# Kernel optimization log

Measured on AMD Instinct MI355X. Metric: run time of the kernel, lower is better.

## Reference

```python
import jax, jax.numpy as jnp
import numpy as np

B, T, D_MEM, D_Q, D_ATT, C_LOC, K = 64, 2000, 512, 1024, 128, 32, 31


def setup_inputs() -> dict:
    key = jax.random.key(0)
    ks = jax.random.split(key, 9)
    return {
        "attention_hidden_state": jax.random.normal(ks[0], (B, 1, D_Q), jnp.float32),
        "memory": jax.random.normal(ks[1], (B, T, D_MEM), jnp.float32),
        "processed_memory": jax.random.normal(ks[2], (B, T, D_ATT), jnp.float32),
        "attention_weights": jax.random.uniform(ks[3], (B, 2, T), jnp.float32),
        "Wq": jax.random.normal(ks[4], (D_Q, D_ATT), jnp.float32) * 0.02,
        "Wconv": jax.random.normal(ks[5], (C_LOC, 2, K), jnp.float32) * 0.1,
        "bconv": jax.random.normal(ks[6], (C_LOC,), jnp.float32) * 0.01,
        "Wloc": jax.random.normal(ks[7], (C_LOC, D_ATT), jnp.float32) * 0.1,
        "v": jax.random.normal(ks[8], (D_ATT,), jnp.float32) * 0.1,
    }


def reference(attention_hidden_state, memory, processed_memory, attention_weights,
              Wq, Wconv, bconv, Wloc, v):
    # query projection: [B,1,1024] @ [1024,128] -> [B,1,128]
    processed_query = jnp.einsum("bqi,io->bqo", attention_hidden_state, Wq)
    # location conv: [B,2,T] -> [B,32,T], 'same' padding (k=31, pad=15)
    loc = jax.lax.conv_general_dilated(
        attention_weights, Wconv, window_strides=(1,), padding=[(15, 15)],
        dimension_numbers=("NCH", "OIH", "NCH"))
    loc = loc + bconv[None, :, None]
    # transpose to [B,T,32] then project to [B,T,128]
    processed_loc = jnp.einsum("bct,co->bto", loc, Wloc)
    # energies: v . tanh(q + loc + mem) -> [B,T]
    energies = jnp.einsum("btd,d->bt", jnp.tanh(processed_query + processed_loc + processed_memory), v)
    new_weights = jax.nn.softmax(energies, axis=1)
    # context: [B,T] x [B,T,D] -> [B,D]
    attention_context = jnp.einsum("bt,btd->bd", new_weights, memory)
    return attention_context, new_weights
```

## Files before the change

kernel.cpp:

```cpp
#include <hip/hip_runtime.h>
#include <hip/hip_bf16.h>

#define B 64
#define T 2000
#define D_MEM 512
#define D_Q 1024
#define D_ATT 128
#define C_LOC 32
#define K 31

#define WS_PQ       0
#define WS_ENERGY   (WS_PQ + B*D_ATT)
#define NCHUNK      20
#define TCHUNK      (T / NCHUNK)
#define WS_PARTIAL  (WS_ENERGY + B*T)

__device__ __forceinline__ float tanh_fast(float x) {
    float e = __expf(2.f * x);
    return 1.f - 2.f / (e + 1.f);
}

__global__ __launch_bounds__(512) void pq_kernel(const float* __restrict__ h,
                                                 const float* __restrict__ Wq,
                                                 float* __restrict__ pq) {
    int b = blockIdx.x;
    int tid = threadIdx.x;
    int ty = tid >> 7;
    int d  = tid & 127;
    __shared__ float sh[D_Q];
    __shared__ float red[4][D_ATT];
    const float* hb = h + (size_t)b * D_Q;
    if (tid < D_Q / 4) ((float4*)sh)[tid] = ((const float4*)hb)[tid];
    __syncthreads();
    float acc = 0.f;
    int ibeg = ty * 256;
#pragma unroll 8
    for (int i2 = 0; i2 < 256; ++i2) {
        int i = ibeg + i2;
        acc = fmaf(sh[i], Wq[(size_t)i * D_ATT + d], acc);
    }
    red[ty][d] = acc;
    __syncthreads();
    if (ty == 0)
        pq[b * D_ATT + d] = red[0][d] + red[1][d] + red[2][d] + red[3][d];
}

#define CH 40
#define TPT 5
__global__ __launch_bounds__(256) void energy_kernel(const float* __restrict__ aw,
                              const float* __restrict__ pmem,
                              const float* __restrict__ pq,
                              const float* __restrict__ Wconv,
                              const float* __restrict__ bconv,
                              const float* __restrict__ Wloc,
                              const float* __restrict__ v,
                              float* __restrict__ energies) {
    const int b  = blockIdx.y;
    const int t0 = blockIdx.x * CH;
    const int tid = threadIdx.x;

    __shared__ float s_aw[2][CH + K - 1];
    __shared__ float s_wc[2 * K * C_LOC];
    __shared__ float s_loc[CH][C_LOC];
    __shared__ float s_pq[D_ATT];

    for (int j = tid; j < 2 * (CH + K - 1); j += 256) {
        int i = j / (CH + K - 1), o = j % (CH + K - 1);
        int t = t0 - (K / 2) + o;
        s_aw[i][o] = (t >= 0 && t < T) ? aw[((size_t)b * 2 + i) * T + t] : 0.f;
    }
    for (int j = tid; j < C_LOC * 2 * K; j += 256) {
        int c = j / (2 * K), r = j % (2 * K);
        int i = r / K, k = r % K;
        s_wc[(i * K + k) * C_LOC + c] = Wconv[j];
    }
    if (tid < D_ATT) s_pq[tid] = pq[b * D_ATT + tid];
    __syncthreads();

    {
        int g = tid >> 5, c = tid & 31;
        float bc = bconv[c];
        float acc[TPT];
#pragma unroll
        for (int j = 0; j < TPT; ++j) acc[j] = bc;
#pragma unroll
        for (int i = 0; i < 2; ++i) {
#pragma unroll
            for (int k = 0; k < K; ++k) {
                float wv = s_wc[(i * K + k) * C_LOC + c];
#pragma unroll
                for (int j = 0; j < TPT; ++j)
                    acc[j] = fmaf(s_aw[i][g + 8 * j + k], wv, acc[j]);
            }
        }
#pragma unroll
        for (int j = 0; j < TPT; ++j) s_loc[g + 8 * j][c] = acc[j];
    }
    __syncthreads();

    int g = tid >> 5, dd = tid & 31;
    float4 pqv = ((const float4*)s_pq)[dd];
    float4 vv  = ((const float4*)v)[dd];
    float4 pl[TPT];
#pragma unroll
    for (int j = 0; j < TPT; ++j) pl[j] = make_float4(0.f, 0.f, 0.f, 0.f);
#pragma unroll
    for (int c = 0; c < C_LOC; ++c) {
        float4 w = ((const float4*)(Wloc + c * D_ATT))[dd];
#pragma unroll
        for (int j = 0; j < TPT; ++j) {
            float l = s_loc[g + 8 * j][c];
            pl[j].x = fmaf(l, w.x, pl[j].x);
            pl[j].y = fmaf(l, w.y, pl[j].y);
            pl[j].z = fmaf(l, w.z, pl[j].z);
            pl[j].w = fmaf(l, w.w, pl[j].w);
        }
    }
#pragma unroll
    for (int j = 0; j < TPT; ++j) {
        int t = t0 + g + 8 * j;
        float4 pm = ((const float4*)(pmem + ((size_t)b * T + t) * D_ATT))[dd];
        float e = vv.x * tanh_fast(pqv.x + pl[j].x + pm.x)
                + vv.y * tanh_fast(pqv.y + pl[j].y + pm.y)
                + vv.z * tanh_fast(pqv.z + pl[j].z + pm.z)
                + vv.w * tanh_fast(pqv.w + pl[j].w + pm.w);
#pragma unroll
        for (int off = 16; off >= 1; off >>= 1)
            e += __shfl_xor(e, off);
        if (dd == 0) energies[(size_t)b * T + t] = e;
    }
}

__global__ __launch_bounds__(256) void softmax_kernel(const float* __restrict__ energies,
                               float* __restrict__ weights) {
    int b = blockIdx.x, tid = threadIdx.x;
    const float* e = energies + (size_t)b * T;
    float vals[8];
    float m = -1e30f;
#pragma unroll
    for (int j = 0; j < 8; ++j) {
        int t = j * 256 + tid;
        vals[j] = (t < T) ? e[t] : -1e30f;
        m = fmaxf(m, vals[j]);
    }
    __shared__ float smax[4], ssum[4];
    int wid = tid >> 6, lane = tid & 63;
#pragma unroll
    for (int off = 32; off >= 1; off >>= 1) m = fmaxf(m, __shfl_xor(m, off));
    if (lane == 0) smax[wid] = m;
    __syncthreads();
    m = fmaxf(fmaxf(smax[0], smax[1]), fmaxf(smax[2], smax[3]));

    float s = 0.f;
#pragma unroll
    for (int j = 0; j < 8; ++j) {
        int t = j * 256 + tid;
        vals[j] = (t < T) ? __expf(vals[j] - m) : 0.f;
        s += vals[j];
    }
#pragma unroll
    for (int off = 32; off >= 1; off >>= 1) s += __shfl_xor(s, off);
    if (lane == 0) ssum[wid] = s;
    __syncthreads();
    s = ssum[0] + ssum[1] + ssum[2] + ssum[3];
    float inv = 1.f / s;
#pragma unroll
    for (int j = 0; j < 8; ++j) {
        int t = j * 256 + tid;
        if (t < T) weights[(size_t)b * T + t] = vals[j] * inv;
    }
}

__global__ __launch_bounds__(128) void ctx_partial_kernel(const float* __restrict__ memory,
                                   const float* __restrict__ weights,
                                   float* __restrict__ partial) {
    int b = blockIdx.y, s = blockIdx.x;
    int dq = threadIdx.x;
    int tbeg = s * TCHUNK;
    __shared__ float sw[TCHUNK];
    const float* w = weights + (size_t)b * T;
    for (int j = threadIdx.x; j < TCHUNK; j += 128) sw[j] = w[tbeg + j];
    __syncthreads();
    const float4* mem4 = (const float4*)(memory + (size_t)b * T * D_MEM);
    float4 acc = {0.f, 0.f, 0.f, 0.f};
#pragma unroll 10
    for (int j = 0; j < TCHUNK; ++j) {
        float wt = sw[j];
        float4 mv = mem4[(size_t)(tbeg + j) * (D_MEM / 4) + dq];
        acc.x = fmaf(wt, mv.x, acc.x);
        acc.y = fmaf(wt, mv.y, acc.y);
        acc.z = fmaf(wt, mv.z, acc.z);
        acc.w = fmaf(wt, mv.w, acc.w);
    }
    ((float4*)(partial + ((size_t)s * B + b) * D_MEM))[dq] = acc;
}

__global__ __launch_bounds__(256) void ctx_reduce_kernel(const float* __restrict__ partial,
                                  float* __restrict__ ctx) {
    int idx = blockIdx.x * 256 + threadIdx.x;
    float acc = 0.f;
#pragma unroll
    for (int s = 0; s < NCHUNK; ++s)
        acc += partial[(size_t)s * B * D_MEM + idx];
    ctx[idx] = acc;
}

extern "C" void kernel_launch(void* const* d_in, const int* in_sizes, int n_in,
                              void* d_out, int out_size, void* d_ws, size_t ws_size,
                              hipStream_t stream) {
    const float* hidden = (const float*)d_in[0];
    const float* memory = (const float*)d_in[1];
    const float* pmem   = (const float*)d_in[2];
    const float* aw     = (const float*)d_in[3];
    const float* Wq     = (const float*)d_in[4];
    const float* Wconv  = (const float*)d_in[5];
    const float* bconv  = (const float*)d_in[6];
    const float* Wloc   = (const float*)d_in[7];
    const float* v      = (const float*)d_in[8];

    float* out_ctx = (float*)d_out;
    float* out_w   = (float*)d_out + B * D_MEM;

    float* ws       = (float*)d_ws;
    float* pq       = ws + WS_PQ;
    float* energies = ws + WS_ENERGY;
    float* partial  = ws + WS_PARTIAL;

    pq_kernel<<<B, 512, 0, stream>>>(hidden, Wq, pq);
    energy_kernel<<<dim3(T / CH, B), 256, 0, stream>>>(aw, pmem, pq, Wconv, bconv,
                                                       Wloc, v, energies);
    softmax_kernel<<<B, 256, 0, stream>>>(energies, out_w);
    ctx_partial_kernel<<<dim3(NCHUNK, B), 128, 0, stream>>>(memory, out_w, partial);
    ctx_reduce_kernel<<<(B * D_MEM) / 256, 256, 0, stream>>>(partial, out_ctx);
}
```

Before: 523.0 us.

## Fuse energy, softmax numerator and context accumulation into one kernel

Merges the energy, softmax and context-partial kernels into one kernel per (batch, 100-step chunk). It computes exp(energy) without subtracting the max, accumulates per-chunk sums and unnormalized context partials, and then normalizes both outputs in a small finalize kernel. This removes the round trips through global memory for energies and weights and cuts the launch count from five to three. In exchange it drops max-subtraction, which risks overflow if energies are large. Larger chunks also mean fewer blocks and heavier per-thread register use.

After: 508.2 us. 2.8% less time.

```diff
diff --git a/kernel.cpp b/kernel.cpp
--- a/kernel.cpp
+++ b/kernel.cpp
@@ -9,11 +9,15 @@
 #define C_LOC 32
 #define K 31
 
-#define WS_PQ       0
-#define WS_ENERGY   (WS_PQ + B*D_ATT)
-#define NCHUNK      20
-#define TCHUNK      (T / NCHUNK)
-#define WS_PARTIAL  (WS_ENERGY + B*T)
+#define CH2 100
+#define NCH2 (T / CH2)
+#define TPG 13
+#define NPART (NCH2 * 2)
+
+#define WS_PQ    0
+#define WS_EXPW  (WS_PQ + B * D_ATT)
+#define WS_SUMS  (WS_EXPW + B * T)
+#define WS_PART  (WS_SUMS + B * NCH2)
 
 __device__ __forceinline__ float tanh_fast(float x) {
     float e = __expf(2.f * x);
@@ -45,33 +49,33 @@
         pq[b * D_ATT + d] = red[0][d] + red[1][d] + red[2][d] + red[3][d];
 }
 
-#define CH 40
-#define TPT 5
-__global__ __launch_bounds__(256) void energy_kernel(const float* __restrict__ aw,
-                              const float* __restrict__ pmem,
-                              const float* __restrict__ pq,
-                              const float* __restrict__ Wconv,
-                              const float* __restrict__ bconv,
-                              const float* __restrict__ Wloc,
-                              const float* __restrict__ v,
-                              float* __restrict__ energies) {
-    const int b  = blockIdx.y;
-    const int t0 = blockIdx.x * CH;
+__global__ __launch_bounds__(256) void mega_kernel(
+    const float* __restrict__ aw, const float* __restrict__ pmem,
+    const float* __restrict__ pq, const float* __restrict__ Wconv,
+    const float* __restrict__ bconv, const float* __restrict__ Wloc,
+    const float* __restrict__ v, const float* __restrict__ memory,
+    float* __restrict__ expw, float* __restrict__ sums,
+    float* __restrict__ partial) {
+    const int s = blockIdx.x, b = blockIdx.y;
+    const int t0 = s * CH2;
     const int tid = threadIdx.x;
 
-    __shared__ float s_aw[2][CH + K - 1];
+    __shared__ float s_aw[2][CH2 + K - 1];
     __shared__ float s_wc[2 * K * C_LOC];
-    __shared__ float s_loc[CH][C_LOC];
+    __shared__ float s_loc[CH2 + 4][C_LOC];
     __shared__ float s_pq[D_ATT];
-
-    for (int j = tid; j < 2 * (CH + K - 1); j += 256) {
-        int i = j / (CH + K - 1), o = j % (CH + K - 1);
+    __shared__ float s_e[CH2];
+    __shared__ float s_red[2];
+
+    const int AWW = CH2 + K - 1;
+    for (int j = tid; j < 2 * AWW; j += 256) {
+        int i = j / AWW, o = j - i * AWW;
         int t = t0 - (K / 2) + o;
         s_aw[i][o] = (t >= 0 && t < T) ? aw[((size_t)b * 2 + i) * T + t] : 0.f;
     }
     for (int j = tid; j < C_LOC * 2 * K; j += 256) {
-        int c = j / (2 * K), r = j % (2 * K);
-        int i = r / K, k = r % K;
+        int c = j / (2 * K), r = j - c * 2 * K;
+        int i = r / K, k = r - i * K;
         s_wc[(i * K + k) * C_LOC + c] = Wconv[j];
     }
     if (tid < D_ATT) s_pq[tid] = pq[b * D_ATT + tid];
@@ -80,129 +84,118 @@
     {
         int g = tid >> 5, c = tid & 31;
         float bc = bconv[c];
-        float acc[TPT];
-#pragma unroll
-        for (int j = 0; j < TPT; ++j) acc[j] = bc;
+        float acc[TPG];
+#pragma unroll
+        for (int j = 0; j < TPG; ++j) acc[j] = bc;
 #pragma unroll
         for (int i = 0; i < 2; ++i) {
 #pragma unroll
             for (int k = 0; k < K; ++k) {
                 float wv = s_wc[(i * K + k) * C_LOC + c];
 #pragma unroll
-                for (int j = 0; j < TPT; ++j)
+                for (int j = 0; j < TPG; ++j)
                     acc[j] = fmaf(s_aw[i][g + 8 * j + k], wv, acc[j]);
             }
         }
 #pragma unroll
-        for (int j = 0; j < TPT; ++j) s_loc[g + 8 * j][c] = acc[j];
-    }
-    __syncthreads();
-
-    int g = tid >> 5, dd = tid & 31;
-    float4 pqv = ((const float4*)s_pq)[dd];
-    float4 vv  = ((const float4*)v)[dd];
-    float4 pl[TPT];
-#pragma unroll
-    for (int j = 0; j < TPT; ++j) pl[j] = make_float4(0.f, 0.f, 0.f, 0.f);
-#pragma unroll
-    for (int c = 0; c < C_LOC; ++c) {
-        float4 w = ((const float4*)(Wloc + c * D_ATT))[dd];
-#pragma unroll
-        for (int j = 0; j < TPT; ++j) {
-            float l = s_loc[g + 8 * j][c];
-            pl[j].x = fmaf(l, w.x, pl[j].x);
-            pl[j].y = fmaf(l, w.y, pl[j].y);
-            pl[j].z = fmaf(l, w.z, pl[j].z);
-            pl[j].w = fmaf(l, w.w, pl[j].w);
-        }
-    }
-#pragma unroll
-    for (int j = 0; j < TPT; ++j) {
-        int t = t0 + g + 8 * j;
-        float4 pm = ((const float4*)(pmem + ((size_t)b * T + t) * D_ATT))[dd];
-        float e = vv.x * tanh_fast(pqv.x + pl[j].x + pm.x)
-                + vv.y * tanh_fast(pqv.y + pl[j].y + pm.y)
-                + vv.z * tanh_fast(pqv.z + pl[j].z + pm.z)
-                + vv.w * tanh_fast(pqv.w + pl[j].w + pm.w);
-#pragma unroll
-        for (int off = 16; off >= 1; off >>= 1)
-            e += __shfl_xor(e, off);
-        if (dd == 0) energies[(size_t)b * T + t] = e;
-    }
-}
-
-__global__ __launch_bounds__(256) void softmax_kernel(const float* __restrict__ energies,
-                               float* __restrict__ weights) {
+        for (int j = 0; j < TPG; ++j) s_loc[g + 8 * j][c] = acc[j];
+    }
+    __syncthreads();
+
+    {
+        int g = tid >> 5, dd = tid & 31;
+        float4 pqv = ((const float4*)s_pq)[dd];
+        float4 vv  = ((const float4*)v)[dd];
+        float4 pl[TPG];
+#pragma unroll
+        for (int j = 0; j < TPG; ++j) pl[j] = make_float4(0.f, 0.f, 0.f, 0.f);
+#pragma unroll
+        for (int c = 0; c < C_LOC; ++c) {
+            float4 w = ((const float4*)(Wloc + c * D_ATT))[dd];
+#pragma unroll
+            for (int j = 0; j < TPG; ++j) {
+                float l = s_loc[g + 8 * j][c];
+                pl[j].x = fmaf(l, w.x, pl[j].x);
+                pl[j].y = fmaf(l, w.y, pl[j].y);
+                pl[j].z = fmaf(l, w.z, pl[j].z);
+                pl[j].w = fmaf(l, w.w, pl[j].w);
+            }
+        }
+#pragma unroll
+        for (int j = 0; j < TPG; ++j) {
+            int tl = g + 8 * j;
+            if (tl < CH2) {
+                int t = t0 + tl;
+                float4 pm = ((const float4*)(pmem + ((size_t)b * T + t) * D_ATT))[dd];
+                float e = vv.x * tanh_fast(pqv.x + pl[j].x + pm.x)
+                        + vv.y * tanh_fast(pqv.y + pl[j].y + pm.y)
+                        + vv.z * tanh_fast(pqv.z + pl[j].z + pm.z)
+                        + vv.w * tanh_fast(pqv.w + pl[j].w + pm.w);
+#pragma unroll
+                for (int off = 16; off >= 1; off >>= 1)
+                    e += __shfl_xor(e, off);
+                if (dd == 0) s_e[tl] = __expf(e);
+            }
+        }
+    }
+    __syncthreads();
+
+    if (tid < 128) {
+        float vsum = (tid < CH2) ? s_e[tid] : 0.f;
+        if (tid < CH2) expw[(size_t)b * T + t0 + tid] = vsum;
+        float r = vsum;
+#pragma unroll
+        for (int off = 32; off >= 1; off >>= 1) r += __shfl_xor(r, off);
+        if ((tid & 63) == 0) s_red[tid >> 6] = r;
+    }
+    __syncthreads();
+    if (tid == 0) sums[b * NCH2 + s] = s_red[0] + s_red[1];
+
+    {
+        int dq = tid & 127, h = tid >> 7;
+        const float4* mem4 =
+            (const float4*)(memory + ((size_t)b * T + t0 + h * 50) * D_MEM);
+        float4 acc = {0.f, 0.f, 0.f, 0.f};
+#pragma unroll 10
+        for (int j = 0; j < 50; ++j) {
+            float wt = s_e[h * 50 + j];
+            float4 mv = mem4[(size_t)j * (D_MEM / 4) + dq];
+            acc.x = fmaf(wt, mv.x, acc.x);
+            acc.y = fmaf(wt, mv.y, acc.y);
+            acc.z = fmaf(wt, mv.z, acc.z);
+            acc.w = fmaf(wt, mv.w, acc.w);
+        }
+        ((float4*)(partial + ((size_t)(s * 2 + h) * B + b) * D_MEM))[dq] = acc;
+    }
+}
+
+__global__ __launch_bounds__(256) void finalize_kernel(
+    const float* __restrict__ expw, const float* __restrict__ sums,
+    const float* __restrict__ partial, float* __restrict__ out_w,
+    float* __restrict__ out_ctx) {
     int b = blockIdx.x, tid = threadIdx.x;
-    const float* e = energies + (size_t)b * T;
-    float vals[8];
-    float m = -1e30f;
-#pragma unroll
-    for (int j = 0; j < 8; ++j) {
-        int t = j * 256 + tid;
-        vals[j] = (t < T) ? e[t] : -1e30f;
-        m = fmaxf(m, vals[j]);
-    }
-    __shared__ float smax[4], ssum[4];
-    int wid = tid >> 6, lane = tid & 63;
-#pragma unroll
-    for (int off = 32; off >= 1; off >>= 1) m = fmaxf(m, __shfl_xor(m, off));
-    if (lane == 0) smax[wid] = m;
-    __syncthreads();
-    m = fmaxf(fmaxf(smax[0], smax[1]), fmaxf(smax[2], smax[3]));
-
-    float s = 0.f;
-#pragma unroll
-    for (int j = 0; j < 8; ++j) {
-        int t = j * 256 + tid;
-        vals[j] = (t < T) ? __expf(vals[j] - m) : 0.f;
-        s += vals[j];
-    }
-#pragma unroll
-    for (int off = 32; off >= 1; off >>= 1) s += __shfl_xor(s, off);
-    if (lane == 0) ssum[wid] = s;
-    __syncthreads();
-    s = ssum[0] + ssum[1] + ssum[2] + ssum[3];
-    float inv = 1.f / s;
-#pragma unroll
-    for (int j = 0; j < 8; ++j) {
-        int t = j * 256 + tid;
-        if (t < T) weights[(size_t)b * T + t] = vals[j] * inv;
-    }
-}
-
-__global__ __launch_bounds__(128) void ctx_partial_kernel(const float* __restrict__ memory,
-                                   const float* __restrict__ weights,
-                                   float* __restrict__ partial) {
-    int b = blockIdx.y, s = blockIdx.x;
-    int dq = threadIdx.x;
-    int tbeg = s * TCHUNK;
-    __shared__ float sw[TCHUNK];
-    const float* w = weights + (size_t)b * T;
-    for (int j = threadIdx.x; j < TCHUNK; j += 128) sw[j] = w[tbeg + j];
-    __syncthreads();
-    const float4* mem4 = (const float4*)(memory + (size_t)b * T * D_MEM);
-    float4 acc = {0.f, 0.f, 0.f, 0.f};
-#pragma unroll 10
-    for (int j = 0; j < TCHUNK; ++j) {
-        float wt = sw[j];
-        float4 mv = mem4[(size_t)(tbeg + j) * (D_MEM / 4) + dq];
-        acc.x = fmaf(wt, mv.x, acc.x);
-        acc.y = fmaf(wt, mv.y, acc.y);
-        acc.z = fmaf(wt, mv.z, acc.z);
-        acc.w = fmaf(wt, mv.w, acc.w);
-    }
-    ((float4*)(partial + ((size_t)s * B + b) * D_MEM))[dq] = acc;
-}
-
-__global__ __launch_bounds__(256) void ctx_reduce_kernel(const float* __restrict__ partial,
-                                  float* __restrict__ ctx) {
-    int idx = blockIdx.x * 256 + threadIdx.x;
-    float acc = 0.f;
-#pragma unroll
-    for (int s = 0; s < NCHUNK; ++s)
-        acc += partial[(size_t)s * B * D_MEM + idx];
-    ctx[idx] = acc;
+    __shared__ float s_inv;
+    if (tid < 64) {
+        float r = (tid < NCH2) ? sums[b * NCH2 + tid] : 0.f;
+#pragma unroll
+        for (int off = 32; off >= 1; off >>= 1) r += __shfl_xor(r, off);
+        if (tid == 0) s_inv = 1.f / r;
+    }
+    __syncthreads();
+    float inv = s_inv;
+    for (int t = tid; t < T; t += 256)
+        out_w[(size_t)b * T + t] = expw[(size_t)b * T + t] * inv;
+    if (tid < 128) {
+        const float4* p4 = (const float4*)partial;
+        float4 acc = {0.f, 0.f, 0.f, 0.f};
+#pragma unroll
+        for (int p = 0; p < NPART; ++p) {
+            float4 pv = p4[((size_t)p * B + b) * (D_MEM / 4) + tid];
+            acc.x += pv.x; acc.y += pv.y; acc.z += pv.z; acc.w += pv.w;
+        }
+        acc.x *= inv; acc.y *= inv; acc.z *= inv; acc.w *= inv;
+        ((float4*)(out_ctx + (size_t)b * D_MEM))[tid] = acc;
+    }
 }
 
 extern "C" void kernel_launch(void* const* d_in, const int* in_sizes, int n_in,
@@ -221,15 +214,15 @@
     float* out_ctx = (float*)d_out;
     float* out_w   = (float*)d_out + B * D_MEM;
 
-    float* ws       = (float*)d_ws;
-    float* pq       = ws + WS_PQ;
-    float* energies = ws + WS_ENERGY;
-    float* partial  = ws + WS_PARTIAL;
-
-    pq_kernel<<<B, 512, 0, stream>>>(hidden, Wq, pq);
-    energy_kernel<<<dim3(T / CH, B), 256, 0, stream>>>(aw, pmem, pq, Wconv, bconv,
-                                                       Wloc, v, energies);
-    softmax_kernel<<<B, 256, 0, stream>>>(energies, out_w);
-    ctx_partial_kernel<<<dim3(NCHUNK, B), 128, 0, stream>>>(memory, out_w, partial);
-    ctx_reduce_kernel<<<(B * D_MEM) / 256, 256, 0, stream>>>(partial, out_ctx);
-}
+    float* ws      = (float*)d_ws;
+    float* pqp     = ws + WS_PQ;
+    float* expw    = ws + WS_EXPW;
+    float* sums    = ws + WS_SUMS;
+    float* partial = ws + WS_PART;
+
+    pq_kernel<<<B, 512, 0, stream>>>(hidden, Wq, pqp);
+    mega_kernel<<<dim3(NCH2, B), 256, 0, stream>>>(aw, pmem, pqp, Wconv, bconv,
+                                                   Wloc, v, memory, expw, sums,
+                                                   partial);
+    finalize_kernel<<<B, 256, 0, stream>>>(expw, sums, partial, out_w, out_ctx);
+}
```
